# Kernel tuning notes

Measured on AMD Instinct MI355X. Metric: run time of the kernel, lower is better.

## Reference

```python
import jax, jax.numpy as jnp
import numpy as np


def setup_inputs() -> dict:
    key = jax.random.key(0)
    k1, k2 = jax.random.split(key)
    B, N, M = 16, 4096, 4096
    points1 = jax.random.normal(k1, (B, N, 3), dtype=jnp.float32)
    points2 = jax.random.normal(k2, (B, M, 3), dtype=jnp.float32)
    return {"points1": points1, "points2": points2}


def reference(points1, points2):
    # Mathematically equal to sum((x - y)^2) without materializing (B,N,M,3).
    w1 = 1.0
    w2 = 1.0
    sq1 = jnp.sum(points1 * points1, axis=-1)  # (B, N)
    sq2 = jnp.sum(points2 * points2, axis=-1)  # (B, M)
    cross = jnp.einsum("bnd,bmd->bnm", points1, points2)  # (B, N, M)
    dist = sq1[:, :, None] + sq2[:, None, :] - 2.0 * cross  # (B, N, M)
    dist_min1 = jnp.min(dist, axis=2)  # nearest in points2 for each point1
    dist_min2 = jnp.min(dist, axis=1)  # nearest in points1 for each point2
    B = points1.shape[0]
    return (w1 * jnp.sum(dist_min1) + w2 * jnp.sum(dist_min2)) / B
```

## Files before the change

kernel.cpp:

```cpp
#include <hip/hip_runtime.h>

typedef _Float16 half8 __attribute__((ext_vector_type(8)));
typedef float f32x16 __attribute__((ext_vector_type(16)));

#define NPTS   4096
#define BATCH  16
#define BLOCK  256
#define CHUNK  2048
#define NCHUNK 2
#define NBLK   1024

__global__ __launch_bounds__(BLOCK, 4) void chamfer_mfma_kernel(
    const float* __restrict__ p1, const float* __restrict__ p2,
    float* __restrict__ partial)
{
    __shared__ half8 REC[CHUNK];

    const int tid  = threadIdx.x;
    const int lane = tid & 63;
    const int n    = lane & 31;
    const int grp  = lane >> 5;
    const int wv   = tid >> 6;
    const int sg   = wv & 1;
    const int oh   = wv >> 1;
    const int blk  = blockIdx.x;
    const int j    = blk & 31;
    const int b    = (blk >> 5) & 15;
    const int dir  = blk >> 9;

    const float* selfp  = (dir == 0 ? p1 : p2) + (size_t)b * NPTS * 3;
    const float* otherp = (dir == 0 ? p2 : p1) + (size_t)b * NPTS * 3;

    const int base = j * 128 + sg * 64;
    half8 a0, a1;
    float ssq01;
    {
        const int i0 = (base + n) * 3, i1 = (base + 32 + n) * 3;
        float x0 = selfp[i0], y0 = selfp[i0 + 1], z0 = selfp[i0 + 2];
        float x1 = selfp[i1], y1 = selfp[i1 + 1], z1 = selfp[i1 + 2];
        ssq01 = fmaf(x0, x0, fmaf(y0, y0, z0 * z0)) +
                fmaf(x1, x1, fmaf(y1, y1, z1 * z1));
        _Float16 hx0 = (_Float16)x0, hy0 = (_Float16)y0, hz0 = (_Float16)z0;
        _Float16 lx0 = (_Float16)(x0 - (float)hx0);
        _Float16 ly0 = (_Float16)(y0 - (float)hy0);
        _Float16 lz0 = (_Float16)(z0 - (float)hz0);
        _Float16 hx1 = (_Float16)x1, hy1 = (_Float16)y1, hz1 = (_Float16)z1;
        _Float16 lx1 = (_Float16)(x1 - (float)hx1);
        _Float16 ly1 = (_Float16)(y1 - (float)hy1);
        _Float16 lz1 = (_Float16)(z1 - (float)hz1);
        const _Float16 c0 = (_Float16)0.f, c1 = (_Float16)1.f;
        if (grp == 0) {
            a0[0]=hx0; a0[1]=hy0; a0[2]=hz0; a0[3]=c0; a0[4]=c0; a0[5]=c0; a0[6]=c1; a0[7]=c0;
            a1[0]=hx1; a1[1]=hy1; a1[2]=hz1; a1[3]=c0; a1[4]=c0; a1[5]=c0; a1[6]=c1; a1[7]=c0;
        } else {
            a0[0]=lx0; a0[1]=ly0; a0[2]=lz0; a0[3]=hx0; a0[4]=hy0; a0[5]=hz0; a0[6]=c0; a0[7]=c1;
            a1[0]=lx1; a1[1]=ly1; a1[2]=lz1; a1[3]=hx1; a1[4]=hy1; a1[5]=hz1; a1[6]=c0; a1[7]=c1;
        }
    }

    f32x16 m0, m1, zc;
#pragma unroll
    for (int r = 0; r < 16; ++r) { m0[r] = 3.4e38f; m1[r] = 3.4e38f; zc[r] = 0.f; }

    for (int c = 0; c < NCHUNK; ++c) {
        __syncthreads();
        {
            const float4* src = (const float4*)(otherp + (size_t)c * CHUNK * 3);
            float4 v0 = src[tid * 6 + 0], v1 = src[tid * 6 + 1];
            float4 v2 = src[tid * 6 + 2], v3 = src[tid * 6 + 3];
            float4 v4 = src[tid * 6 + 4], v5 = src[tid * 6 + 5];
            float ox[8] = {v0.x, v0.w, v1.z, v2.y, v3.x, v3.w, v4.z, v5.y};
            float oy[8] = {v0.y, v1.x, v1.w, v2.z, v3.y, v4.x, v4.w, v5.z};
            float oz[8] = {v0.z, v1.y, v2.x, v2.w, v3.z, v4.y, v5.x, v5.w};
#pragma unroll
            for (int k = 0; k < 8; ++k) {
                float gx = -2.f * ox[k], gy = -2.f * oy[k], gz = -2.f * oz[k];
                float q  = fmaf(ox[k], ox[k], fmaf(oy[k], oy[k], oz[k] * oz[k]));
                _Float16 ghx = (_Float16)gx, ghy = (_Float16)gy, ghz = (_Float16)gz;
                half8 r;
                r[0] = ghx; r[1] = ghy; r[2] = ghz;
                r[3] = (_Float16)(gx - (float)ghx);
                r[4] = (_Float16)(gy - (float)ghy);
                r[5] = (_Float16)(gz - (float)ghz);
                _Float16 qh = (_Float16)q;
                r[6] = qh;
                r[7] = (_Float16)(q - (float)qh);
                REC[tid * 8 + k] = r;
            }
        }
        __syncthreads();
        const half8* rp = REC + oh * (CHUNK / 2) + n;
#pragma unroll 2
        for (int g = 0; g < CHUNK / 2 / 64; ++g) {
            half8 b0 = rp[g * 64];
            half8 b1 = rp[g * 64 + 32];
            f32x16 o00 = __builtin_amdgcn_mfma_f32_32x32x16_f16(a0, b0, zc, 0, 0, 0);
            f32x16 o01 = __builtin_amdgcn_mfma_f32_32x32x16_f16(a0, b1, zc, 0, 0, 0);
            f32x16 o10 = __builtin_amdgcn_mfma_f32_32x32x16_f16(a1, b0, zc, 0, 0, 0);
            f32x16 o11 = __builtin_amdgcn_mfma_f32_32x32x16_f16(a1, b1, zc, 0, 0, 0);
#pragma unroll
            for (int r = 0; r < 16; ++r) {
                m0[r] = fminf(fminf(o00[r], o01[r]), m0[r]);
                m1[r] = fminf(fminf(o10[r], o11[r]), m1[r]);
            }
        }
    }

    __syncthreads();
    float* CW = (float*)REC;
    if (oh == 1) {
#pragma unroll
        for (int r = 0; r < 16; ++r) {
            CW[((sg * 2 + 0) * 64 + lane) * 17 + r] = m0[r];
            CW[((sg * 2 + 1) * 64 + lane) * 17 + r] = m1[r];
        }
    }
    __syncthreads();
    if (oh == 0) {
#pragma unroll
        for (int r = 0; r < 16; ++r) {
            m0[r] = fminf(m0[r], CW[((sg * 2 + 0) * 64 + lane) * 17 + r]);
            m1[r] = fminf(m1[r], CW[((sg * 2 + 1) * 64 + lane) * 17 + r]);
        }
#pragma unroll
        for (int mask = 1; mask <= 16; mask <<= 1) {
#pragma unroll
            for (int r = 0; r < 16; ++r) {
                m0[r] = fminf(m0[r], __shfl_xor((float)m0[r], mask, 64));
                m1[r] = fminf(m1[r], __shfl_xor((float)m1[r], mask, 64));
            }
        }
        float rowsum = 0.f;
#pragma unroll
        for (int r = 0; r < 16; ++r) rowsum += m0[r] + m1[r];
        rowsum += __shfl_xor(rowsum, 32, 64);

        float sv = grp ? 0.f : ssq01;
#pragma unroll
        for (int mask = 1; mask <= 16; mask <<= 1)
            sv += __shfl_xor(sv, mask, 64);

        if (lane == 0) partial[blk * 2 + sg] = rowsum + sv;
    }
}

__global__ __launch_bounds__(256) void chamfer_reduce(
    const float* __restrict__ partial, float* __restrict__ out)
{
    float s = 0.f;
    for (int i = threadIdx.x; i < NBLK * 2; i += 256) s += partial[i];
#pragma unroll
    for (int off = 32; off > 0; off >>= 1) s += __shfl_down(s, off, 64);
    __shared__ float ws4[4];
    int lane = threadIdx.x & 63, wv = threadIdx.x >> 6;
    if (lane == 0) ws4[wv] = s;
    __syncthreads();
    if (threadIdx.x == 0)
        out[0] = (ws4[0] + ws4[1] + ws4[2] + ws4[3]) * (1.0f / BATCH);
}

extern "C" void kernel_launch(void* const* d_in, const int* in_sizes, int n_in,
                              void* d_out, int out_size, void* d_ws, size_t ws_size,
                              hipStream_t stream) {
    const float* p1 = (const float*)d_in[0];
    const float* p2 = (const float*)d_in[1];
    float* out = (float*)d_out;
    float* partial = (float*)d_ws;

    chamfer_mfma_kernel<<<dim3(NBLK), dim3(BLOCK), 0, stream>>>(p1, p2, partial);
    chamfer_reduce<<<dim3(1), dim3(256), 0, stream>>>(partial, out);
}
```

Measured before the change: 81.99 us.

## Switch to 16x16x32 MFMA with eight row fragments per wave

Replaces the 32x32x16 f16 MFMA tiling with the 16x16x32 variant. Each wave now holds 8 row fragments covering all 128 self points and walks its own quarter of the other-point chunk, so the work split changes from row halves to column quarters. The final reduction now combines four per-wave column mins through shared memory and writes one partial per block. Half of each K=32 fragment is zero padding, so the MFMAs carry twice the nominal work, in exchange for more independent MFMAs per loaded B fragment and a simpler epilogue.

```diff
diff --git a/kernel.cpp b/kernel.cpp
--- a/kernel.cpp
+++ b/kernel.cpp
@@ -1,7 +1,7 @@
 #include <hip/hip_runtime.h>
 
 typedef _Float16 half8 __attribute__((ext_vector_type(8)));
-typedef float f32x16 __attribute__((ext_vector_type(16)));
+typedef float f32x4 __attribute__((ext_vector_type(4)));
 
 #define NPTS   4096
 #define BATCH  16
@@ -9,6 +9,7 @@
 #define CHUNK  2048
 #define NCHUNK 2
 #define NBLK   1024
+#define NFRAG  8
 
 __global__ __launch_bounds__(BLOCK, 4) void chamfer_mfma_kernel(
     const float* __restrict__ p1, const float* __restrict__ p2,
@@ -18,11 +19,9 @@
 
     const int tid  = threadIdx.x;
     const int lane = tid & 63;
-    const int n    = lane & 31;
-    const int grp  = lane >> 5;
+    const int n    = lane & 15;
+    const int quad = lane >> 4;
     const int wv   = tid >> 6;
-    const int sg   = wv & 1;
-    const int oh   = wv >> 1;
     const int blk  = blockIdx.x;
     const int j    = blk & 31;
     const int b    = (blk >> 5) & 15;
@@ -31,36 +30,36 @@
     const float* selfp  = (dir == 0 ? p1 : p2) + (size_t)b * NPTS * 3;
     const float* otherp = (dir == 0 ? p2 : p1) + (size_t)b * NPTS * 3;
 
-    const int base = j * 128 + sg * 64;
-    half8 a0, a1;
-    float ssq01;
+    half8 af[NFRAG];
     {
-        const int i0 = (base + n) * 3, i1 = (base + 32 + n) * 3;
-        float x0 = selfp[i0], y0 = selfp[i0 + 1], z0 = selfp[i0 + 2];
-        float x1 = selfp[i1], y1 = selfp[i1 + 1], z1 = selfp[i1 + 2];
-        ssq01 = fmaf(x0, x0, fmaf(y0, y0, z0 * z0)) +
-                fmaf(x1, x1, fmaf(y1, y1, z1 * z1));
-        _Float16 hx0 = (_Float16)x0, hy0 = (_Float16)y0, hz0 = (_Float16)z0;
-        _Float16 lx0 = (_Float16)(x0 - (float)hx0);
-        _Float16 ly0 = (_Float16)(y0 - (float)hy0);
-        _Float16 lz0 = (_Float16)(z0 - (float)hz0);
-        _Float16 hx1 = (_Float16)x1, hy1 = (_Float16)y1, hz1 = (_Float16)z1;
-        _Float16 lx1 = (_Float16)(x1 - (float)hx1);
-        _Float16 ly1 = (_Float16)(y1 - (float)hy1);
-        _Float16 lz1 = (_Float16)(z1 - (float)hz1);
         const _Float16 c0 = (_Float16)0.f, c1 = (_Float16)1.f;
-        if (grp == 0) {
-            a0[0]=hx0; a0[1]=hy0; a0[2]=hz0; a0[3]=c0; a0[4]=c0; a0[5]=c0; a0[6]=c1; a0[7]=c0;
-            a1[0]=hx1; a1[1]=hy1; a1[2]=hz1; a1[3]=c0; a1[4]=c0; a1[5]=c0; a1[6]=c1; a1[7]=c0;
-        } else {
-            a0[0]=lx0; a0[1]=ly0; a0[2]=lz0; a0[3]=hx0; a0[4]=hy0; a0[5]=hz0; a0[6]=c0; a0[7]=c1;
-            a1[0]=lx1; a1[1]=ly1; a1[2]=lz1; a1[3]=hx1; a1[4]=hy1; a1[5]=hz1; a1[6]=c0; a1[7]=c1;
+#pragma unroll
+        for (int f = 0; f < NFRAG; ++f) {
+            const int i0 = (j * 128 + f * 16 + n) * 3;
+            float x = selfp[i0], y = selfp[i0 + 1], z = selfp[i0 + 2];
+            _Float16 hx = (_Float16)x, hy = (_Float16)y, hz = (_Float16)z;
+            half8 a;
+            if (quad == 0) {
+                a[0] = hx; a[1] = hy; a[2] = hz;
+                a[3] = c0; a[4] = c0; a[5] = c0; a[6] = c1; a[7] = c0;
+            } else if (quad == 1) {
+                a[0] = (_Float16)(x - (float)hx);
+                a[1] = (_Float16)(y - (float)hy);
+                a[2] = (_Float16)(z - (float)hz);
+                a[3] = hx; a[4] = hy; a[5] = hz; a[6] = c0; a[7] = c1;
+            } else {
+                a[0]=c0; a[1]=c0; a[2]=c0; a[3]=c0;
+                a[4]=c0; a[5]=c0; a[6]=c0; a[7]=c0;
+            }
+            af[f] = a;
         }
     }
 
-    f32x16 m0, m1, zc;
+    f32x4 m[NFRAG];
+    f32x4 zc = {0.f, 0.f, 0.f, 0.f};
 #pragma unroll
-    for (int r = 0; r < 16; ++r) { m0[r] = 3.4e38f; m1[r] = 3.4e38f; zc[r] = 0.f; }
+    for (int f = 0; f < NFRAG; ++f)
+        m[f] = (f32x4){3.4e38f, 3.4e38f, 3.4e38f, 3.4e38f};
 
     for (int c = 0; c < NCHUNK; ++c) {
         __syncthreads();
@@ -89,66 +88,63 @@
             }
         }
         __syncthreads();
-        const half8* rp = REC + oh * (CHUNK / 2) + n;
+        const half8* rp = REC + wv * 512 + n;
 #pragma unroll 2
-        for (int g = 0; g < CHUNK / 2 / 64; ++g) {
-            half8 b0 = rp[g * 64];
-            half8 b1 = rp[g * 64 + 32];
-            f32x16 o00 = __builtin_amdgcn_mfma_f32_32x32x16_f16(a0, b0, zc, 0, 0, 0);
-            f32x16 o01 = __builtin_amdgcn_mfma_f32_32x32x16_f16(a0, b1, zc, 0, 0, 0);
-            f32x16 o10 = __builtin_amdgcn_mfma_f32_32x32x16_f16(a1, b0, zc, 0, 0, 0);
-            f32x16 o11 = __builtin_amdgcn_mfma_f32_32x32x16_f16(a1, b1, zc, 0, 0, 0);
+        for (int t = 0; t < 16; ++t) {
+            half8 b0 = rp[(2 * t + 0) * 16];
+            half8 b1 = rp[(2 * t + 1) * 16];
 #pragma unroll
-            for (int r = 0; r < 16; ++r) {
-                m0[r] = fminf(fminf(o00[r], o01[r]), m0[r]);
-                m1[r] = fminf(fminf(o10[r], o11[r]), m1[r]);
+            for (int f = 0; f < NFRAG; ++f) {
+                f32x4 o0 = __builtin_amdgcn_mfma_f32_16x16x32_f16(af[f], b0, zc, 0, 0, 0);
+                f32x4 o1 = __builtin_amdgcn_mfma_f32_16x16x32_f16(af[f], b1, zc, 0, 0, 0);
+#pragma unroll
+                for (int r = 0; r < 4; ++r)
+                    m[f][r] = fminf(fminf(o0[r], o1[r]), m[f][r]);
             }
         }
     }
 
+#pragma unroll
+    for (int mask = 1; mask <= 8; mask <<= 1) {
+#pragma unroll
+        for (int f = 0; f < NFRAG; ++f)
+#pragma unroll
+            for (int r = 0; r < 4; ++r)
+                m[f][r] = fminf(m[f][r], __shfl_xor((float)m[f][r], mask, 64));
+    }
     __syncthreads();
     float* CW = (float*)REC;
-    if (oh == 1) {
+    if (n == 0) {
 #pragma unroll
-        for (int r = 0; r < 16; ++r) {
-            CW[((sg * 2 + 0) * 64 + lane) * 17 + r] = m0[r];
-            CW[((sg * 2 + 1) * 64 + lane) * 17 + r] = m1[r];
-        }
+        for (int f = 0; f < NFRAG; ++f)
+#pragma unroll
+            for (int r = 0; r < 4; ++r)
+                CW[wv * 136 + f * 16 + quad * 4 + r] = m[f][r];
     }
     __syncthreads();
-    if (oh == 0) {
+
+    float d = 0.f;
+    if (tid < 128) {
+        float mn = fminf(fminf(CW[tid], CW[136 + tid]),
+                         fminf(CW[272 + tid], CW[408 + tid]));
+        const int i0 = (j * 128 + tid) * 3;
+        float x = selfp[i0], y = selfp[i0 + 1], z = selfp[i0 + 2];
+        d = fmaf(x, x, fmaf(y, y, z * z)) + mn;
+    }
 #pragma unroll
-        for (int r = 0; r < 16; ++r) {
-            m0[r] = fminf(m0[r], CW[((sg * 2 + 0) * 64 + lane) * 17 + r]);
-            m1[r] = fminf(m1[r], CW[((sg * 2 + 1) * 64 + lane) * 17 + r]);
-        }
-#pragma unroll
-        for (int mask = 1; mask <= 16; mask <<= 1) {
-#pragma unroll
-            for (int r = 0; r < 16; ++r) {
-                m0[r] = fminf(m0[r], __shfl_xor((float)m0[r], mask, 64));
-                m1[r] = fminf(m1[r], __shfl_xor((float)m1[r], mask, 64));
-            }
-        }
-        float rowsum = 0.f;
-#pragma unroll
-        for (int r = 0; r < 16; ++r) rowsum += m0[r] + m1[r];
-        rowsum += __shfl_xor(rowsum, 32, 64);
-
-        float sv = grp ? 0.f : ssq01;
-#pragma unroll
-        for (int mask = 1; mask <= 16; mask <<= 1)
-            sv += __shfl_xor(sv, mask, 64);
-
-        if (lane == 0) partial[blk * 2 + sg] = rowsum + sv;
-    }
+    for (int off = 32; off > 0; off >>= 1) d += __shfl_down(d, off, 64);
+    __shared__ float ws4[4];
+    if (lane == 0) ws4[wv] = d;
+    __syncthreads();
+    if (tid == 0)
+        partial[blk] = ws4[0] + ws4[1] + ws4[2] + ws4[3];
 }
 
 __global__ __launch_bounds__(256) void chamfer_reduce(
     const float* __restrict__ partial, float* __restrict__ out)
 {
     float s = 0.f;
-    for (int i = threadIdx.x; i < NBLK * 2; i += 256) s += partial[i];
+    for (int i = threadIdx.x; i < NBLK; i += 256) s += partial[i];
 #pragma unroll
     for (int off = 32; off > 0; off >>= 1) s += __shfl_down(s, off, 64);
     __shared__ float ws4[4];
```

Result: slower. 88.88 us (+8.4%).
